# Kernel optimization log

Hardware: AMD Instinct MI355X
Metric: run time of the kernel (lower is better)

## Reference

```python
import jax, jax.numpy as jnp
import numpy as np
import math

B, S, D, H = 2, 4096, 512, 8
DK = D // H


def setup_inputs() -> dict:
    key = jax.random.key(0)
    ks = jax.random.split(key, 9)
    s = 1.0 / math.sqrt(D)
    return {
        "x": jax.random.normal(ks[0], (B, S, D), dtype=jnp.float32),
        "Wq": jax.random.normal(ks[1], (D, D), dtype=jnp.float32) * s,
        "bq": jax.random.normal(ks[2], (D,), dtype=jnp.float32) * 0.01,
        "Wk": jax.random.normal(ks[3], (D, D), dtype=jnp.float32) * s,
        "bk": jax.random.normal(ks[4], (D,), dtype=jnp.float32) * 0.01,
        "Wv": jax.random.normal(ks[5], (D, D), dtype=jnp.float32) * s,
        "bv": jax.random.normal(ks[6], (D,), dtype=jnp.float32) * 0.01,
        "Wo": jax.random.normal(ks[7], (D, D), dtype=jnp.float32) * s,
        "bo": jax.random.normal(ks[8], (D,), dtype=jnp.float32) * 0.01,
    }


def reference(x, Wq, bq, Wk, bk, Wv, bv, Wo, bo):
    b, s, _ = x.shape
    # projections, split into heads: (b, h, s, dk)
    def proj(W, bias):
        return (x @ W.T + bias).reshape(b, s, H, DK).transpose(0, 2, 1, 3)
    Q, K, V = proj(Wq, bq), proj(Wk, bk), proj(Wv, bv)
    scale = 1.0 / math.sqrt(DK)
    scores = jnp.einsum("bhqd,bhkd->bhqk", Q, K) * scale  # (b,h,s,s)
    causal = jnp.tril(jnp.ones((s, s), dtype=bool))
    scores = jnp.where(causal[None, None], scores, -jnp.inf)
    attn = jax.nn.softmax(scores, axis=-1)
    out = jnp.einsum("bhqk,bhkd->bhqd", attn, V)
    out = out.transpose(0, 2, 1, 3).reshape(b, s, D)
    return out @ Wo.T + bo
```

## Files before the change

kernel.cpp:

```cpp
#include <hip/hip_runtime.h>
#include <hip/hip_bf16.h>

using u16    = unsigned short;
using u32    = unsigned int;
using bf16x8 = __attribute__((ext_vector_type(8))) __bf16;
using s16x4  = __attribute__((ext_vector_type(4))) short;
using f32x4  = __attribute__((ext_vector_type(4))) float;
using u16x4  = __attribute__((ext_vector_type(4))) unsigned short;
using u16x8  = __attribute__((ext_vector_type(8))) unsigned short;
using u32x2  = __attribute__((ext_vector_type(2))) unsigned int;
using u32x4  = __attribute__((ext_vector_type(4))) unsigned int;


static __device__ __forceinline__ u16 f2bf(float f) {
  unsigned int u = __float_as_uint(f);
  u += 0x7fffu + ((u >> 16) & 1u);
  return (u16)(u >> 16);
}
static __device__ __forceinline__ u32 pack2bf(float lo, float hi) {
  return __builtin_amdgcn_perm(__float_as_uint(hi), __float_as_uint(lo), 0x07060302u);
}

__global__ __launch_bounds__(256) void cvt_all(
    const float* __restrict__ x,  const float* __restrict__ wq,
    const float* __restrict__ wk, const float* __restrict__ wv,
    const float* __restrict__ wo,
    u16* __restrict__ xb, u16* __restrict__ wqb, u16* __restrict__ wkb,
    u16* __restrict__ wvb, u16* __restrict__ wob) {
  const int bx = blockIdx.x;
  const float* src;
  u16* dst;
  int i;
  if (bx < 4096) {
    src = x; dst = xb; i = bx * 256 + threadIdx.x;
  } else {
    const int t  = (bx - 4096) >> 8;
    const int lb = (bx - 4096) & 255;
    src = (t == 0) ? wq : (t == 1) ? wk : (t == 2) ? wv : wo;
    dst = (t == 0) ? wqb : (t == 1) ? wkb : (t == 2) ? wvb : wob;
    i = lb * 256 + threadIdx.x;
  }
  float4 v = reinterpret_cast<const float4*>(src)[i];
  u16x4 o = { f2bf(v.x), f2bf(v.y), f2bf(v.z), f2bf(v.w) };
  reinterpret_cast<u16x4*>(dst)[i] = o;
}

__global__ __launch_bounds__(256, 3) void gemm_qkv(const u16* __restrict__ A,
                                                   const u16* __restrict__ Wq,
                                                   const u16* __restrict__ Wk,
                                                   const u16* __restrict__ Wv,
                                                   const float* __restrict__ bqp,
                                                   const float* __restrict__ bkp,
                                                   const float* __restrict__ bvp,
                                                   u16* __restrict__ Qo,
                                                   u16* __restrict__ Ko,
                                                   u16* __restrict__ Vto) {
  const int which = blockIdx.z;
  const u16* W = (which == 0) ? Wq : (which == 1) ? Wk : Wv;
  const float* bias = (which == 0) ? bqp : (which == 1) ? bkp : bvp;

  __shared__ u16 sA[128 * 72];
  __shared__ u16 sB[128 * 72];
  const int row0 = blockIdx.x * 128;
  const int col0 = blockIdx.y * 128;
  const int tid  = threadIdx.x;
  const int lane = tid & 63;
  const int wave = tid >> 6;
  const int wm   = (wave & 1) * 64;
  const int wn   = (wave >> 1) * 64;
  const int ln   = lane & 15;
  const int quad = lane >> 4;

  int rr[4], cc[4];
  for (int i = 0; i < 4; ++i) {
    const int idx = tid + 256 * i;
    rr[i] = idx >> 3; cc[i] = (idx & 7) * 8;
  }

  f32x4 zero = {0.f, 0.f, 0.f, 0.f};
  f32x4 acc[4][4];
  for (int i = 0; i < 4; ++i)
    for (int j = 0; j < 4; ++j) acc[i][j] = zero;

  u16x8 curA[4], nxtA[4];
  for (int i = 0; i < 4; ++i)
    curA[i] = *reinterpret_cast<const u16x8*>(&A[(row0 + rr[i]) * 512 + cc[i]]);

  for (int k0 = 0; k0 < 512; k0 += 64) {
    __syncthreads();
    for (int i = 0; i < 4; ++i) {
      *reinterpret_cast<u16x8*>(&sA[rr[i] * 72 + cc[i]]) = curA[i];
      *reinterpret_cast<u16x8*>(&sB[rr[i] * 72 + cc[i]]) =
          *reinterpret_cast<const u16x8*>(&W[(col0 + rr[i]) * 512 + k0 + cc[i]]);
    }
    if (k0 < 448)
      for (int i = 0; i < 4; ++i)
        nxtA[i] = *reinterpret_cast<const u16x8*>(&A[(row0 + rr[i]) * 512 + k0 + 64 + cc[i]]);
    __syncthreads();
    for (int ks = 0; ks < 2; ++ks) {
      bf16x8 af[4], bfr[4];
      for (int t4 = 0; t4 < 4; ++t4)
        af[t4] = *reinterpret_cast<const bf16x8*>(&sA[(wm + t4 * 16 + ln) * 72 + ks * 32 + quad * 8]);
      for (int t4 = 0; t4 < 4; ++t4)
        bfr[t4] = *reinterpret_cast<const bf16x8*>(&sB[(wn + t4 * 16 + ln) * 72 + ks * 32 + quad * 8]);
      for (int tm = 0; tm < 4; ++tm)
        for (int tn = 0; tn < 4; ++tn)
          acc[tm][tn] = __builtin_amdgcn_mfma_f32_16x16x32_bf16(af[tm], bfr[tn], acc[tm][tn], 0, 0, 0);
    }
    for (int i = 0; i < 4; ++i) curA[i] = nxtA[i];
  }

  if (which < 2) {
    u16* out = (which == 0) ? Qo : Ko;
    const float scale = (which == 0) ? 0.125f : 1.0f;
    for (int tm = 0; tm < 4; ++tm) {
      const int mbase = row0 + wm + tm * 16 + quad * 4;
      for (int tn = 0; tn < 4; ++tn) {
        const int n  = col0 + wn + tn * 16 + ln;
        const int h  = n >> 6, dk = n & 63;
        const float bv = bias[n];
        for (int r = 0; r < 4; ++r) {
          const int m  = mbase + r;
          const int bh = ((m >> 12) << 3) + h;
          const int s  = m & 4095;
          out[(bh * 4096 + s) * 64 + dk] = f2bf((acc[tm][tn][r] + bv) * scale);
        }
      }
    }
  } else {
    for (int tm = 0; tm < 4; ++tm) {
      const int mbase = row0 + wm + tm * 16 + quad * 4;
      const int b_idx = mbase >> 12;
      const int s     = mbase & 4095;
      for (int tn = 0; tn < 4; ++tn) {
        const int n  = col0 + wn + tn * 16 + ln;
        const int h  = n >> 6, dk = n & 63;
        const int bh = b_idx * 8 + h;
        const float bv = bias[n];
        u16x4 o;
        for (int r = 0; r < 4; ++r) o[r] = f2bf(acc[tm][tn][r] + bv);
        *reinterpret_cast<u16x4*>(&Vto[(bh * 64 + dk) * 4096 + s]) = o;
      }
    }
  }
}

__global__ __launch_bounds__(256, 4) void gemm_out(const u16* __restrict__ A,
                                                   const u16* __restrict__ W,
                                                   const float* __restrict__ bias,
                                                   float* __restrict__ out) {
  __shared__ u16 sA[64 * 72];
  __shared__ u16 sB[128 * 72];
  const int row0 = blockIdx.x * 64;
  const int col0 = blockIdx.y * 128;
  const int tid  = threadIdx.x;
  const int lane = tid & 63;
  const int wave = tid >> 6;
  const int wm   = (wave & 1) * 32;
  const int wn   = (wave >> 1) * 64;
  const int ln   = lane & 15;
  const int quad = lane >> 4;

  int rr[4], cc[4];
  for (int i = 0; i < 4; ++i) {
    const int idx = tid + 256 * i;
    rr[i] = idx >> 3; cc[i] = (idx & 7) * 8;
  }

  f32x4 zero = {0.f, 0.f, 0.f, 0.f};
  f32x4 acc[2][4];
  for (int i = 0; i < 2; ++i)
    for (int j = 0; j < 4; ++j) acc[i][j] = zero;

  u16x8 curA[2], nxtA[2];
  for (int i = 0; i < 2; ++i)
    curA[i] = *reinterpret_cast<const u16x8*>(&A[(row0 + rr[i]) * 512 + cc[i]]);

  for (int k0 = 0; k0 < 512; k0 += 64) {
    __syncthreads();
    for (int i = 0; i < 2; ++i)
      *reinterpret_cast<u16x8*>(&sA[rr[i] * 72 + cc[i]]) = curA[i];
    for (int i = 0; i < 4; ++i)
      *reinterpret_cast<u16x8*>(&sB[rr[i] * 72 + cc[i]]) =
          *reinterpret_cast<const u16x8*>(&W[(col0 + rr[i]) * 512 + k0 + cc[i]]);
    if (k0 < 448)
      for (int i = 0; i < 2; ++i)
        nxtA[i] = *reinterpret_cast<const u16x8*>(&A[(row0 + rr[i]) * 512 + k0 + 64 + cc[i]]);
    __syncthreads();
    for (int ks = 0; ks < 2; ++ks) {
      bf16x8 af[2], bfr[4];
      for (int t4 = 0; t4 < 2; ++t4)
        af[t4] = *reinterpret_cast<const bf16x8*>(&sA[(wm + t4 * 16 + ln) * 72 + ks * 32 + quad * 8]);
      for (int t4 = 0; t4 < 4; ++t4)
        bfr[t4] = *reinterpret_cast<const bf16x8*>(&sB[(wn + t4 * 16 + ln) * 72 + ks * 32 + quad * 8]);
      for (int tm = 0; tm < 2; ++tm)
        for (int tn = 0; tn < 4; ++tn)
          acc[tm][tn] = __builtin_amdgcn_mfma_f32_16x16x32_bf16(af[tm], bfr[tn], acc[tm][tn], 0, 0, 0);
    }
    for (int i = 0; i < 2; ++i) curA[i] = nxtA[i];
  }

  for (int tm = 0; tm < 2; ++tm) {
    const int mbase = row0 + wm + tm * 16 + quad * 4;
    for (int tn = 0; tn < 4; ++tn) {
      const int n  = col0 + wn + tn * 16 + ln;
      const float bv = bias[n];
      for (int r = 0; r < 4; ++r)
        out[(mbase + r) * 512 + n] = acc[tm][tn][r] + bv;
    }
  }
}

#if __has_builtin(__builtin_amdgcn_mfma_f32_16x16x16bf16_1k)
#define HAVE_MFMA16 1
#endif
__global__ __launch_bounds__(256, 4) void attn_part(const u16* __restrict__ Q,
                                                    const u16* __restrict__ K,
                                                    const u16* __restrict__ Vt,
                                                    float* __restrict__ pO,
                                                    float* __restrict__ pl) {
  const int c = blockIdx.x;
  const int t = blockIdx.y;
  const int g = t >> 2;
  if (c > g) return;
  const int ktlast = 2 * t + 1;
  const int kt0 = 8 * c;
  const int kt1 = (kt0 + 7 < ktlast) ? (kt0 + 7) : ktlast;
  const int bh = blockIdx.z;
  const int qb = t * 128;

  const u16* Qh  = Q  + bh * 4096 * 64;
  const u16* Kh  = K  + bh * 4096 * 64;
  const u16* Vth = Vt + bh * 64 * 4096;

  __shared__ u16 sK[2][64 * 72];
  __shared__ u16 sV[2][64 * 72];

  const int tid  = threadIdx.x;
  const int lane = tid & 63;
  const int wave = tid >> 6;
  const int ln   = lane & 15;
  const int quad = lane >> 4;

  const int r0 = tid >> 3,         c0 = (tid & 7) * 8;
  const int r1 = (tid + 256) >> 3, c1 = ((tid + 256) & 7) * 8;

  bf16x8 qf[2][2];
  for (int tn = 0; tn < 2; ++tn)
    for (int ks = 0; ks < 2; ++ks)
      qf[tn][ks] = *reinterpret_cast<const bf16x8*>(
          &Qh[(qb + wave * 32 + tn * 16 + ln) * 64 + ks * 32 + quad * 8]);

  f32x4 zero = {0.f, 0.f, 0.f, 0.f};
  f32x4 accO[4][2];
  float lsum[2] = {0.f, 0.f};
  for (int td = 0; td < 4; ++td)
    for (int tn = 0; tn < 2; ++tn) accO[td][tn] = zero;

#ifndef HAVE_MFMA16
  const int idx0 = 4 * (ln + 16 * (2 * (quad & 1)));
#endif

  u16x8 cur[4], nxt[4];
  {
    const int kb = kt0 * 64;
    cur[0] = *reinterpret_cast<const u16x8*>(&Kh[(kb + r0) * 64 + c0]);
    cur[1] = *reinterpret_cast<const u16x8*>(&Kh[(kb + r1) * 64 + c1]);
    cur[2] = *reinterpret_cast<const u16x8*>(&Vth[r0 * 4096 + kb + c0]);
    cur[3] = *reinterpret_cast<const u16x8*>(&Vth[r1 * 4096 + kb + c1]);
    *reinterpret_cast<u16x8*>(&sK[0][r0 * 72 + c0]) = cur[0];
    *reinterpret_cast<u16x8*>(&sK[0][r1 * 72 + c1]) = cur[1];
    *reinterpret_cast<u16x8*>(&sV[0][r0 * 72 + c0]) = cur[2];
    *reinterpret_cast<u16x8*>(&sV[0][r1 * 72 + c1]) = cur[3];
    const int kn = kb + 64;
    cur[0] = *reinterpret_cast<const u16x8*>(&Kh[(kn + r0) * 64 + c0]);
    cur[1] = *reinterpret_cast<const u16x8*>(&Kh[(kn + r1) * 64 + c1]);
    cur[2] = *reinterpret_cast<const u16x8*>(&Vth[r0 * 4096 + kn + c0]);
    cur[3] = *reinterpret_cast<const u16x8*>(&Vth[r1 * 4096 + kn + c1]);
  }

  int pb = 0;
  for (int kt = kt0; kt <= kt1; ++kt) {
    const int kb = kt * 64;
    __syncthreads();
    if (kt < kt1) {
      u16* dK = sK[pb ^ 1];
      u16* dV = sV[pb ^ 1];
      *reinterpret_cast<u16x8*>(&dK[r0 * 72 + c0]) = cur[0];
      *reinterpret_cast<u16x8*>(&dK[r1 * 72 + c1]) = cur[1];
      *reinterpret_cast<u16x8*>(&dV[r0 * 72 + c0]) = cur[2];
      *reinterpret_cast<u16x8*>(&dV[r1 * 72 + c1]) = cur[3];
      if (kt + 2 <= kt1) {
        const int kn = kb + 128;
        nxt[0] = *reinterpret_cast<const u16x8*>(&Kh[(kn + r0) * 64 + c0]);
        nxt[1] = *reinterpret_cast<const u16x8*>(&Kh[(kn + r1) * 64 + c1]);
        nxt[2] = *reinterpret_cast<const u16x8*>(&Vth[r0 * 4096 + kn + c0]);
        nxt[3] = *reinterpret_cast<const u16x8*>(&Vth[r1 * 4096 + kn + c1]);
      }
    }
    const u16* bK = sK[pb];
    const u16* bV = sV[pb];

    f32x4 accS[4][2];
    for (int tm = 0; tm < 4; ++tm)
      for (int tn = 0; tn < 2; ++tn) accS[tm][tn] = zero;
    for (int tm = 0; tm < 4; ++tm) {
      bf16x8 kf0 = *reinterpret_cast<const bf16x8*>(&bK[(tm * 16 + ln) * 72 + quad * 8]);
      bf16x8 kf1 = *reinterpret_cast<const bf16x8*>(&bK[(tm * 16 + ln) * 72 + 32 + quad * 8]);
      for (int tn = 0; tn < 2; ++tn) {
        accS[tm][tn] = __builtin_amdgcn_mfma_f32_16x16x32_bf16(kf0, qf[tn][0], accS[tm][tn], 0, 0, 0);
        accS[tm][tn] = __builtin_amdgcn_mfma_f32_16x16x32_bf16(kf1, qf[tn][1], accS[tm][tn], 0, 0, 0);
      }
    }

    const bool diag = (kt >= 2 * t);
    u32 pp[4][2][2];
    for (int tm = 0; tm < 4; ++tm)
      for (int tn = 0; tn < 2; ++tn) {
        f32x4 e = accS[tm][tn];
        if (diag) {
          const int kg = kb + tm * 16 + quad * 4;
          const int qg = qb + wave * 32 + tn * 16 + ln;
          for (int r = 0; r < 4; ++r)
            if (kg + r > qg) e[r] = -__builtin_inff();
        }
        for (int r = 0; r < 4; ++r) e[r] = __expf(e[r]);
        lsum[tn] += (e[0] + e[1]) + (e[2] + e[3]);
        pp[tm][tn][0] = pack2bf(e[0], e[1]);
        pp[tm][tn][1] = pack2bf(e[2], e[3]);
      }

#ifdef HAVE_MFMA16
    for (int k16 = 0; k16 < 4; ++k16)
      for (int td = 0; td < 4; ++td) {
        s16x4 vf = *reinterpret_cast<const s16x4*>(&bV[(td * 16 + ln) * 72 + k16 * 16 + quad * 4]);
        for (int tn = 0; tn < 2; ++tn) {
          u32x2 pr = { pp[k16][tn][0], pp[k16][tn][1] };
          s16x4 pbv = __builtin_bit_cast(s16x4, pr);
          accO[td][tn] = __builtin_amdgcn_mfma_f32_16x16x16bf16_1k(vf, pbv, accO[td][tn], 0, 0, 0);
        }
      }
#else
    for (int ks = 0; ks < 2; ++ks)
      for (int tn = 0; tn < 2; ++tn) {
        u32 b[4];
        for (int half = 0; half < 2; ++half)
          for (int p = 0; p < 2; ++p) {
            int v0 = __builtin_amdgcn_ds_bpermute(idx0 + 64 * half, (int)pp[2 * ks][tn][p]);
            int v1 = __builtin_amdgcn_ds_bpermute(idx0 + 64 * half, (int)pp[2 * ks + 1][tn][p]);
            b[half * 2 + p] = (quad < 2) ? (u32)v0 : (u32)v1;
          }
        u32x4 bv4 = { b[0], b[1], b[2], b[3] };
        bf16x8 pfrag = __builtin_bit_cast(bf16x8, bv4);
        for (int td = 0; td < 4; ++td) {
          bf16x8 vf = *reinterpret_cast<const bf16x8*>(&bV[(td * 16 + ln) * 72 + ks * 32 + quad * 8]);
          accO[td][tn] = __builtin_amdgcn_mfma_f32_16x16x32_bf16(vf, pfrag, accO[td][tn], 0, 0, 0);
        }
      }
#endif
    for (int j = 0; j < 4; ++j) cur[j] = nxt[j];
    pb ^= 1;
  }

  for (int tn = 0; tn < 2; ++tn) {
    lsum[tn] += __shfl_xor(lsum[tn], 16);
    lsum[tn] += __shfl_xor(lsum[tn], 32);
  }
  const int slot = bh * 144 + t + 2 * g * (g - 1) + (t & 3) * g + c;
  float* po = pO + (size_t)slot * 8192;
  for (int td = 0; td < 4; ++td)
    for (int tn = 0; tn < 2; ++tn)
      for (int r = 0; r < 4; ++r)
        po[(td * 16 + quad * 4 + r) * 128 + wave * 32 + tn * 16 + ln] = accO[td][tn][r];
  if (quad == 0)
    for (int tn = 0; tn < 2; ++tn)
      pl[slot * 128 + wave * 32 + tn * 16 + ln] = lsum[tn];
}

__global__ __launch_bounds__(256) void attn_comb(const float* __restrict__ pO,
                                                 const float* __restrict__ pl,
                                                 u16* __restrict__ ctx) {
  const int t  = blockIdx.x;
  const int bh = blockIdx.y;
  const int g  = t >> 2;
  const int nch = g + 1;
  const int base = bh * 144 + t + 2 * g * (g - 1) + (t & 3) * g;
  const int tid = threadIdx.x;

  __shared__ float sO[64 * 132];
  __shared__ float sL[128];

  float4 acc[8];
  for (int i = 0; i < 8; ++i) acc[i] = make_float4(0.f, 0.f, 0.f, 0.f);
  float lacc = 0.f;
  for (int cidx = 0; cidx < nch; ++cidx) {
    const float* src = pO + (size_t)(base + cidx) * 8192;
    for (int i = 0; i < 8; ++i) {
      float4 v = reinterpret_cast<const float4*>(src)[i * 256 + tid];
      acc[i].x += v.x; acc[i].y += v.y; acc[i].z += v.z; acc[i].w += v.w;
    }
    if (tid < 128) lacc += pl[(base + cidx) * 128 + tid];
  }
  for (int i = 0; i < 8; ++i) {
    const int f = i * 256 + tid;
    const int d = f >> 5, q = (f & 31) * 4;
    *reinterpret_cast<float4*>(&sO[d * 132 + q]) = acc[i];
  }
  if (tid < 128) sL[tid] = lacc;
  __syncthreads();

  const int q  = tid >> 1;
  const int d0 = (tid & 1) * 32;
  const float inv = 1.0f / sL[q];
  const int b_idx = bh >> 3, h = bh & 7;
  const int tok = (b_idx << 12) + t * 128 + q;
  u16* dst = &ctx[tok * 512 + h * 64 + d0];
  for (int gI = 0; gI < 4; ++gI) {
    u16x8 ov;
    for (int j = 0; j < 8; ++j) ov[j] = f2bf(sO[(d0 + gI * 8 + j) * 132 + q] * inv);
    *reinterpret_cast<u16x8*>(&dst[gI * 8]) = ov;
  }
}

extern "C" void kernel_launch(void* const* d_in, const int* in_sizes, int n_in,
                              void* d_out, int out_size, void* d_ws, size_t ws_size,
                              hipStream_t stream) {
  const float* x  = (const float*)d_in[0];
  const float* Wq = (const float*)d_in[1];
  const float* bq = (const float*)d_in[2];
  const float* Wk = (const float*)d_in[3];
  const float* bk = (const float*)d_in[4];
  const float* Wv = (const float*)d_in[5];
  const float* bv = (const float*)d_in[6];
  const float* Wo = (const float*)d_in[7];
  const float* bo = (const float*)d_in[8];
  float* out = (float*)d_out;

  char* ws = (char*)d_ws;
  u16* xb  = (u16*)(ws + 0);
  u16* wqb = (u16*)(ws + 8388608);
  u16* wkb = (u16*)(ws + 8912896);
  u16* wvb = (u16*)(ws + 9437184);
  u16* wob = (u16*)(ws + 9961472);
  u16* Qb  = (u16*)(ws + 10485760);
  u16* Kb  = (u16*)(ws + 18874368);
  u16* Vtb = (u16*)(ws + 27262976);
  float* pO = (float*)(ws + 35651584);
  float* pl = (float*)(ws + 111149056);
  u16* ctx = xb;

  cvt_all<<<5120, 256, 0, stream>>>(x, Wq, Wk, Wv, Wo, xb, wqb, wkb, wvb, wob);
  gemm_qkv<<<dim3(64, 4, 3), 256, 0, stream>>>(xb, wqb, wkb, wvb, bq, bk, bv, Qb, Kb, Vtb);
  attn_part<<<dim3(8, 32, 16), 256, 0, stream>>>(Qb, Kb, Vtb, pO, pl);
  attn_comb<<<dim3(32, 16), 256, 0, stream>>>(pO, pl, ctx);
  gemm_out<<<dim3(128, 4), 256, 0, stream>>>(ctx, wob, bo, out);
}
```

Before: 209.7 us.

## Store K/V in MFMA fragment order and load directly to registers, bf16 partials

The QKV GEMM epilogue now writes K and V in a pre-swizzled layout matching the MFMA operand fragments, so the attention kernel loads K and V fragments straight from global memory into registers. This removes the shared-memory staging, double buffering and __syncthreads in the KV loop. The partial output buffer is also stored as bf16 instead of fp32, halving that traffic in the partial and combine kernels. Occupancy hint drops to 2 blocks per SU because of extra register use, and bf16 partials add rounding error before the sum.

```diff
diff --git a/kernel.cpp b/kernel.cpp
--- a/kernel.cpp
+++ b/kernel.cpp
@@ -16,6 +16,9 @@
   unsigned int u = __float_as_uint(f);
   u += 0x7fffu + ((u >> 16) & 1u);
   return (u16)(u >> 16);
+}
+static __device__ __forceinline__ float bf2f(u16 v) {
+  return __uint_as_float(((u32)v) << 16);
 }
 static __device__ __forceinline__ u32 pack2bf(float lo, float hi) {
   return __builtin_amdgcn_perm(__float_as_uint(hi), __float_as_uint(lo), 0x07060302u);
@@ -53,8 +56,8 @@
                                                    const float* __restrict__ bkp,
                                                    const float* __restrict__ bvp,
                                                    u16* __restrict__ Qo,
-                                                   u16* __restrict__ Ko,
-                                                   u16* __restrict__ Vto) {
+                                                   u16* __restrict__ Kfo,
+                                                   u16* __restrict__ Vfo) {
   const int which = blockIdx.z;
   const u16* W = (which == 0) ? Wq : (which == 1) ? Wk : Wv;
   const float* bias = (which == 0) ? bqp : (which == 1) ? bkp : bvp;
@@ -110,9 +113,7 @@
     for (int i = 0; i < 4; ++i) curA[i] = nxtA[i];
   }
 
-  if (which < 2) {
-    u16* out = (which == 0) ? Qo : Ko;
-    const float scale = (which == 0) ? 0.125f : 1.0f;
+  if (which == 0) {
     for (int tm = 0; tm < 4; ++tm) {
       const int mbase = row0 + wm + tm * 16 + quad * 4;
       for (int tn = 0; tn < 4; ++tn) {
@@ -123,23 +124,43 @@
           const int m  = mbase + r;
           const int bh = ((m >> 12) << 3) + h;
           const int s  = m & 4095;
-          out[(bh * 4096 + s) * 64 + dk] = f2bf((acc[tm][tn][r] + bv) * scale);
+          Qo[(bh * 4096 + s) * 64 + dk] = f2bf((acc[tm][tn][r] + bv) * 0.125f);
         }
+      }
+    }
+  } else if (which == 1) {
+    for (int tm = 0; tm < 4; ++tm) {
+      const int mbase = row0 + wm + tm * 16 + quad * 4;
+      const int b_idx = mbase >> 12;
+      const int sb    = mbase & 4095;
+      const int kt = sb >> 6, tmk = (sb >> 4) & 3, lnk = sb & 15;
+      for (int tn = 0; tn < 4; ++tn) {
+        const int n  = col0 + wn + tn * 16 + ln;
+        const int h  = n >> 6, dk = n & 63;
+        const int ks = dk >> 5, qd = (dk >> 3) & 3, j = dk & 7;
+        const int bh = b_idx * 8 + h;
+        const float bv = bias[n];
+        u16* dst = &Kfo[(size_t)(bh * 64 + kt) * 4096 + (size_t)(((tmk * 2 + ks) * 64 + qd * 16 + lnk) * 8 + j)];
+        for (int r = 0; r < 4; ++r)
+          dst[r * 8] = f2bf(acc[tm][tn][r] + bv);
       }
     }
   } else {
     for (int tm = 0; tm < 4; ++tm) {
       const int mbase = row0 + wm + tm * 16 + quad * 4;
       const int b_idx = mbase >> 12;
-      const int s     = mbase & 4095;
+      const int sb    = mbase & 4095;
+      const int kt = sb >> 6, k16 = (sb >> 4) & 3, qd = (sb >> 2) & 3;
       for (int tn = 0; tn < 4; ++tn) {
         const int n  = col0 + wn + tn * 16 + ln;
-        const int h  = n >> 6, dk = n & 63;
+        const int h  = n >> 6, d = n & 63;
+        const int td = d >> 4, lnv = d & 15;
         const int bh = b_idx * 8 + h;
         const float bv = bias[n];
         u16x4 o;
         for (int r = 0; r < 4; ++r) o[r] = f2bf(acc[tm][tn][r] + bv);
-        *reinterpret_cast<u16x4*>(&Vto[(bh * 64 + dk) * 4096 + s]) = o;
+        *reinterpret_cast<u16x4*>(
+            &Vfo[(size_t)(bh * 64 + kt) * 4096 + (size_t)(((k16 * 4 + td) * 64 + qd * 16 + lnv) * 4)]) = o;
       }
     }
   }
@@ -214,10 +235,10 @@
 #if __has_builtin(__builtin_amdgcn_mfma_f32_16x16x16bf16_1k)
 #define HAVE_MFMA16 1
 #endif
-__global__ __launch_bounds__(256, 4) void attn_part(const u16* __restrict__ Q,
-                                                    const u16* __restrict__ K,
-                                                    const u16* __restrict__ Vt,
-                                                    float* __restrict__ pO,
+__global__ __launch_bounds__(256, 2) void attn_part(const u16* __restrict__ Q,
+                                                    const u16* __restrict__ Kf,
+                                                    const u16* __restrict__ Vf,
+                                                    u16* __restrict__ pO,
                                                     float* __restrict__ pl) {
   const int c = blockIdx.x;
   const int t = blockIdx.y;
@@ -229,12 +250,9 @@
   const int bh = blockIdx.z;
   const int qb = t * 128;
 
-  const u16* Qh  = Q  + bh * 4096 * 64;
-  const u16* Kh  = K  + bh * 4096 * 64;
-  const u16* Vth = Vt + bh * 64 * 4096;
-
-  __shared__ u16 sK[2][64 * 72];
-  __shared__ u16 sV[2][64 * 72];
+  const u16* Qh = Q  + (size_t)bh * 4096 * 64;
+  const u16* Kb = Kf + (size_t)bh * 64 * 4096;
+  const u16* Vb = Vf + (size_t)bh * 64 * 4096;
 
   const int tid  = threadIdx.x;
   const int lane = tid & 63;
@@ -242,9 +260,6 @@
   const int ln   = lane & 15;
   const int quad = lane >> 4;
 
-  const int r0 = tid >> 3,         c0 = (tid & 7) * 8;
-  const int r1 = (tid + 256) >> 3, c1 = ((tid + 256) & 7) * 8;
-
   bf16x8 qf[2][2];
   for (int tn = 0; tn < 2; ++tn)
     for (int ks = 0; ks < 2; ++ks)
@@ -261,57 +276,51 @@
   const int idx0 = 4 * (ln + 16 * (2 * (quad & 1)));
 #endif
 
-  u16x8 cur[4], nxt[4];
+  bf16x8 kfc[4][2], kfn[4][2];
   {
-    const int kb = kt0 * 64;
-    cur[0] = *reinterpret_cast<const u16x8*>(&Kh[(kb + r0) * 64 + c0]);
-    cur[1] = *reinterpret_cast<const u16x8*>(&Kh[(kb + r1) * 64 + c1]);
-    cur[2] = *reinterpret_cast<const u16x8*>(&Vth[r0 * 4096 + kb + c0]);
-    cur[3] = *reinterpret_cast<const u16x8*>(&Vth[r1 * 4096 + kb + c1]);
-    *reinterpret_cast<u16x8*>(&sK[0][r0 * 72 + c0]) = cur[0];
-    *reinterpret_cast<u16x8*>(&sK[0][r1 * 72 + c1]) = cur[1];
-    *reinterpret_cast<u16x8*>(&sV[0][r0 * 72 + c0]) = cur[2];
-    *reinterpret_cast<u16x8*>(&sV[0][r1 * 72 + c1]) = cur[3];
-    const int kn = kb + 64;
-    cur[0] = *reinterpret_cast<const u16x8*>(&Kh[(kn + r0) * 64 + c0]);
-    cur[1] = *reinterpret_cast<const u16x8*>(&Kh[(kn + r1) * 64 + c1]);
-    cur[2] = *reinterpret_cast<const u16x8*>(&Vth[r0 * 4096 + kn + c0]);
-    cur[3] = *reinterpret_cast<const u16x8*>(&Vth[r1 * 4096 + kn + c1]);
-  }
-
-  int pb = 0;
+    const u16* kp = Kb + kt0 * 4096;
+    for (int tm = 0; tm < 4; ++tm)
+      for (int ks = 0; ks < 2; ++ks)
+        kfc[tm][ks] = *reinterpret_cast<const bf16x8*>(&kp[((tm * 2 + ks) * 64 + lane) * 8]);
+  }
+
   for (int kt = kt0; kt <= kt1; ++kt) {
     const int kb = kt * 64;
-    __syncthreads();
+    const u16* vp = Vb + kt * 4096;
+
+#ifdef HAVE_MFMA16
+    u16x4 vfc[4][4];
+    for (int k16 = 0; k16 < 4; ++k16)
+      for (int td = 0; td < 4; ++td)
+        vfc[k16][td] = *reinterpret_cast<const u16x4*>(&vp[((k16 * 4 + td) * 64 + lane) * 4]);
+#else
+    bf16x8 vfx[4][2];
+    for (int td = 0; td < 4; ++td)
+      for (int ks = 0; ks < 2; ++ks) {
+        const int k16a = 2 * ks + (quad >> 1);
+        const int qa   = (quad & 1) * 2;
+        u16x4 lo = *reinterpret_cast<const u16x4*>(&vp[((k16a * 4 + td) * 64 + qa * 16 + ln) * 4]);
+        u16x4 hi = *reinterpret_cast<const u16x4*>(&vp[((k16a * 4 + td) * 64 + (qa + 1) * 16 + ln) * 4]);
+        u16x8 cm = { lo[0], lo[1], lo[2], lo[3], hi[0], hi[1], hi[2], hi[3] };
+        vfx[td][ks] = __builtin_bit_cast(bf16x8, cm);
+      }
+#endif
+
     if (kt < kt1) {
-      u16* dK = sK[pb ^ 1];
-      u16* dV = sV[pb ^ 1];
-      *reinterpret_cast<u16x8*>(&dK[r0 * 72 + c0]) = cur[0];
-      *reinterpret_cast<u16x8*>(&dK[r1 * 72 + c1]) = cur[1];
-      *reinterpret_cast<u16x8*>(&dV[r0 * 72 + c0]) = cur[2];
-      *reinterpret_cast<u16x8*>(&dV[r1 * 72 + c1]) = cur[3];
-      if (kt + 2 <= kt1) {
-        const int kn = kb + 128;
-        nxt[0] = *reinterpret_cast<const u16x8*>(&Kh[(kn + r0) * 64 + c0]);
-        nxt[1] = *reinterpret_cast<const u16x8*>(&Kh[(kn + r1) * 64 + c1]);
-        nxt[2] = *reinterpret_cast<const u16x8*>(&Vth[r0 * 4096 + kn + c0]);
-        nxt[3] = *reinterpret_cast<const u16x8*>(&Vth[r1 * 4096 + kn + c1]);
-      }
-    }
-    const u16* bK = sK[pb];
-    const u16* bV = sV[pb];
+      const u16* kp = Kb + (kt + 1) * 4096;
+      for (int tm = 0; tm < 4; ++tm)
+        for (int ks = 0; ks < 2; ++ks)
+          kfn[tm][ks] = *reinterpret_cast<const bf16x8*>(&kp[((tm * 2 + ks) * 64 + lane) * 8]);
+    }
 
     f32x4 accS[4][2];
     for (int tm = 0; tm < 4; ++tm)
       for (int tn = 0; tn < 2; ++tn) accS[tm][tn] = zero;
-    for (int tm = 0; tm < 4; ++tm) {
-      bf16x8 kf0 = *reinterpret_cast<const bf16x8*>(&bK[(tm * 16 + ln) * 72 + quad * 8]);
-      bf16x8 kf1 = *reinterpret_cast<const bf16x8*>(&bK[(tm * 16 + ln) * 72 + 32 + quad * 8]);
+    for (int tm = 0; tm < 4; ++tm)
       for (int tn = 0; tn < 2; ++tn) {
-        accS[tm][tn] = __builtin_amdgcn_mfma_f32_16x16x32_bf16(kf0, qf[tn][0], accS[tm][tn], 0, 0, 0);
-        accS[tm][tn] = __builtin_amdgcn_mfma_f32_16x16x32_bf16(kf1, qf[tn][1], accS[tm][tn], 0, 0, 0);
-      }
-    }
+        accS[tm][tn] = __builtin_amdgcn_mfma_f32_16x16x32_bf16(kfc[tm][0], qf[tn][0], accS[tm][tn], 0, 0, 0);
+        accS[tm][tn] = __builtin_amdgcn_mfma_f32_16x16x32_bf16(kfc[tm][1], qf[tn][1], accS[tm][tn], 0, 0, 0);
+      }
 
     const bool diag = (kt >= 2 * t);
     u32 pp[4][2][2];
@@ -333,11 +342,11 @@
 #ifdef HAVE_MFMA16
     for (int k16 = 0; k16 < 4; ++k16)
       for (int td = 0; td < 4; ++td) {
-        s16x4 vf = *reinterpret_cast<const s16x4*>(&bV[(td * 16 + ln) * 72 + k16 * 16 + quad * 4]);
+        s16x4 vv = __builtin_bit_cast(s16x4, vfc[k16][td]);
         for (int tn = 0; tn < 2; ++tn) {
           u32x2 pr = { pp[k16][tn][0], pp[k16][tn][1] };
           s16x4 pbv = __builtin_bit_cast(s16x4, pr);
-          accO[td][tn] = __builtin_amdgcn_mfma_f32_16x16x16bf16_1k(vf, pbv, accO[td][tn], 0, 0, 0);
+          accO[td][tn] = __builtin_amdgcn_mfma_f32_16x16x16bf16_1k(vv, pbv, accO[td][tn], 0, 0, 0);
         }
       }
 #else
@@ -352,14 +361,12 @@
           }
         u32x4 bv4 = { b[0], b[1], b[2], b[3] };
         bf16x8 pfrag = __builtin_bit_cast(bf16x8, bv4);
-        for (int td = 0; td < 4; ++td) {
-          bf16x8 vf = *reinterpret_cast<const bf16x8*>(&bV[(td * 16 + ln) * 72 + ks * 32 + quad * 8]);
-          accO[td][tn] = __builtin_amdgcn_mfma_f32_16x16x32_bf16(vf, pfrag, accO[td][tn], 0, 0, 0);
-        }
+        for (int td = 0; td < 4; ++td)
+          accO[td][tn] = __builtin_amdgcn_mfma_f32_16x16x32_bf16(vfx[td][ks], pfrag, accO[td][tn], 0, 0, 0);
       }
 #endif
-    for (int j = 0; j < 4; ++j) cur[j] = nxt[j];
-    pb ^= 1;
+    for (int tm = 0; tm < 4; ++tm)
+      for (int ks = 0; ks < 2; ++ks) kfc[tm][ks] = kfn[tm][ks];
   }
 
   for (int tn = 0; tn < 2; ++tn) {
@@ -367,17 +374,17 @@
     lsum[tn] += __shfl_xor(lsum[tn], 32);
   }
   const int slot = bh * 144 + t + 2 * g * (g - 1) + (t & 3) * g + c;
-  float* po = pO + (size_t)slot * 8192;
+  u16* po = pO + (size_t)slot * 8192;
   for (int td = 0; td < 4; ++td)
     for (int tn = 0; tn < 2; ++tn)
       for (int r = 0; r < 4; ++r)
-        po[(td * 16 + quad * 4 + r) * 128 + wave * 32 + tn * 16 + ln] = accO[td][tn][r];
+        po[(td * 16 + quad * 4 + r) * 128 + wave * 32 + tn * 16 + ln] = f2bf(accO[td][tn][r]);
   if (quad == 0)
     for (int tn = 0; tn < 2; ++tn)
       pl[slot * 128 + wave * 32 + tn * 16 + ln] = lsum[tn];
 }
 
-__global__ __launch_bounds__(256) void attn_comb(const float* __restrict__ pO,
+__global__ __launch_bounds__(256) void attn_comb(const u16* __restrict__ pO,
                                                  const float* __restrict__ pl,
                                                  u16* __restrict__ ctx) {
   const int t  = blockIdx.x;
@@ -390,21 +397,23 @@
   __shared__ float sO[64 * 132];
   __shared__ float sL[128];
 
-  float4 acc[8];
-  for (int i = 0; i < 8; ++i) acc[i] = make_float4(0.f, 0.f, 0.f, 0.f);
+  float acc[4][8];
+  for (int i = 0; i < 4; ++i)
+    for (int j = 0; j < 8; ++j) acc[i][j] = 0.f;
   float lacc = 0.f;
   for (int cidx = 0; cidx < nch; ++cidx) {
-    const float* src = pO + (size_t)(base + cidx) * 8192;
-    for (int i = 0; i < 8; ++i) {
-      float4 v = reinterpret_cast<const float4*>(src)[i * 256 + tid];
-      acc[i].x += v.x; acc[i].y += v.y; acc[i].z += v.z; acc[i].w += v.w;
+    const u16* src = pO + (size_t)(base + cidx) * 8192;
+    for (int i = 0; i < 4; ++i) {
+      u16x8 v = reinterpret_cast<const u16x8*>(src)[i * 256 + tid];
+      for (int j = 0; j < 8; ++j) acc[i][j] += bf2f(v[j]);
     }
     if (tid < 128) lacc += pl[(base + cidx) * 128 + tid];
   }
-  for (int i = 0; i < 8; ++i) {
-    const int f = i * 256 + tid;
-    const int d = f >> 5, q = (f & 31) * 4;
-    *reinterpret_cast<float4*>(&sO[d * 132 + q]) = acc[i];
+  for (int i = 0; i < 4; ++i) {
+    const int f = (i * 256 + tid) * 8;
+    const int d = f >> 7, q = f & 127;
+    *reinterpret_cast<float4*>(&sO[d * 132 + q])     = make_float4(acc[i][0], acc[i][1], acc[i][2], acc[i][3]);
+    *reinterpret_cast<float4*>(&sO[d * 132 + q + 4]) = make_float4(acc[i][4], acc[i][5], acc[i][6], acc[i][7]);
   }
   if (tid < 128) sL[tid] = lacc;
   __syncthreads();
@@ -443,15 +452,15 @@
   u16* wvb = (u16*)(ws + 9437184);
   u16* wob = (u16*)(ws + 9961472);
   u16* Qb  = (u16*)(ws + 10485760);
-  u16* Kb  = (u16*)(ws + 18874368);
-  u16* Vtb = (u16*)(ws + 27262976);
-  float* pO = (float*)(ws + 35651584);
-  float* pl = (float*)(ws + 111149056);
+  u16* Kfb = (u16*)(ws + 18874368);
+  u16* Vfb = (u16*)(ws + 27262976);
+  u16* pO  = (u16*)(ws + 35651584);
+  float* pl = (float*)(ws + 73400320);
   u16* ctx = xb;
 
   cvt_all<<<5120, 256, 0, stream>>>(x, Wq, Wk, Wv, Wo, xb, wqb, wkb, wvb, wob);
-  gemm_qkv<<<dim3(64, 4, 3), 256, 0, stream>>>(xb, wqb, wkb, wvb, bq, bk, bv, Qb, Kb, Vtb);
-  attn_part<<<dim3(8, 32, 16), 256, 0, stream>>>(Qb, Kb, Vtb, pO, pl);
+  gemm_qkv<<<dim3(64, 4, 3), 256, 0, stream>>>(xb, wqb, wkb, wvb, bq, bk, bv, Qb, Kfb, Vfb);
+  attn_part<<<dim3(8, 32, 16), 256, 0, stream>>>(Qb, Kfb, Vfb, pO, pl);
   attn_comb<<<dim3(32, 16), 256, 0, stream>>>(pO, pl, ctx);
   gemm_out<<<dim3(128, 4), 256, 0, stream>>>(ctx, wob, bo, out);
 }
```

New measurement: 230.0 us. 9.7% more time.
